# Performance work log

Measured on AMD Instinct MI355X. Metric: run time of the kernel, lower is better.

## Reference

```python
import jax, jax.numpy as jnp
import numpy as np
from jax import lax

EPS = 1e-5


def maxpool3x3(x):
    # 3x3 max pool, stride 1, pad 1 (NCHW)
    return lax.reduce_window(x, -jnp.inf, lax.max,
                             window_dimensions=(1, 1, 3, 3),
                             window_strides=(1, 1, 1, 1),
                             padding=((0, 0), (0, 0), (1, 1), (1, 1)))


def focus_downsample(x):
    B, C, H, W = x.shape
    pad_h = (3 - H % 3) % 3
    pad_w = (3 - W % 3) % 3
    if pad_h or pad_w:
        x = jnp.pad(x, ((0, 0), (0, 0), (0, pad_h), (0, pad_w)))
    return jnp.concatenate([x[..., i::3, j::3] for i in range(3) for j in range(3)], axis=1)


def batchnorm(x, gamma, beta):
    # training-mode BatchNorm2d: stats over (B,H,W)
    mean = jnp.mean(x, axis=(0, 2, 3), keepdims=True)
    var = jnp.var(x, axis=(0, 2, 3), keepdims=True)
    g = gamma.reshape(1, -1, 1, 1)
    b = beta.reshape(1, -1, 1, 1)
    return (x - mean) * jax.lax.rsqrt(var + EPS) * g + b


def dwconv(x, w, pad_h, pad_w):
    # depthwise conv, w: (C,1,kh,kw)
    return lax.conv_general_dilated(x, w, window_strides=(1, 1),
                                    padding=((pad_h, pad_h), (pad_w, pad_w)),
                                    dimension_numbers=('NCHW', 'OIHW', 'NCHW'),
                                    feature_group_count=x.shape[1])


def h_transform(x):
    B, C, H, W = x.shape
    x = jnp.pad(x, ((0, 0), (0, 0), (0, 0), (0, W)))
    x = x.reshape(B, C, -1)[..., :-W]
    return x.reshape(B, C, H, 2 * W - 1)


def inv_h_transform(x):
    B, C, H, _ = x.shape
    x = x.reshape(B, C, -1)
    x = jnp.pad(x, ((0, 0), (0, 0), (0, H)))
    x = x.reshape(B, C, H, 2 * H)
    return x[..., :H]


def v_transform(x):
    return h_transform(x.transpose(0, 1, 3, 2)).transpose(0, 1, 3, 2)


def inv_v_transform(x):
    return inv_h_transform(x.transpose(0, 1, 3, 2)).transpose(0, 1, 3, 2)


def pixel_shuffle3(x):
    B, C9, h, w = x.shape
    C = C9 // 9
    x = x.reshape(B, C, 3, 3, h, w)
    x = x.transpose(0, 1, 4, 2, 5, 3)  # B,C,h,3,w,3
    return x.reshape(B, C, 3 * h, 3 * w)


def setup_inputs() -> dict:
    key = jax.random.key(0)
    ks = jax.random.split(key, 10)
    C, K = 64, 11
    B, H, W = 16, 144, 144
    s = 0.05
    return {
        'x': jax.random.normal(ks[0], (B, C, H, W), jnp.float32),
        'w_mixer': jax.random.normal(ks[1], (9, C, C), jnp.float32) * s,
        'g_mnorm': jnp.ones((9 * C,), jnp.float32),
        'b_mnorm': jnp.zeros((9 * C,), jnp.float32),
        'w_h1': jax.random.normal(ks[2], (C, 1, K, 3), jnp.float32) * s,
        'w_v1': jax.random.normal(ks[3], (C, 1, 3, K), jnp.float32) * s,
        'w_h2': jax.random.normal(ks[4], (C, 1, K, 3), jnp.float32) * s,
        'w_v2': jax.random.normal(ks[5], (C, 1, 3, K), jnp.float32) * s,
        'g_norm': jnp.ones((C,), jnp.float32),
        'b_norm': jnp.zeros((C,), jnp.float32),
    }


def reference(x, w_mixer, g_mnorm, b_mnorm, w_h1, w_v1, w_h2, w_v2, g_norm, b_norm):
    C = w_h1.shape[0]
    K = w_h1.shape[2]
    pad = K // 2
    H, W = x.shape[-2:]

    x_pool = maxpool3x3(x)
    x_focus = focus_downsample(x_pool)               # (B,9C,H/3,W/3)

    # grouped 1x1 conv, groups=9
    B, _, h, w = x_focus.shape
    xg = x_focus.reshape(B, 9, C, h, w)
    x_mixed = jnp.einsum('goi,bgihw->bgohw', w_mixer, xg).reshape(B, 9 * C, h, w)
    x_mixed = batchnorm(x_mixed, g_mnorm, b_mnorm)

    x_tem, x_key = x_mixed[:, :C], x_mixed[:, C:]

    x_h1 = dwconv(x_tem, w_h1, pad, 1)
    x_w1 = dwconv(x_tem, w_v1, 1, pad)
    x_h2 = inv_h_transform(dwconv(h_transform(x_tem), w_h2, pad, 1))
    x_w2 = inv_v_transform(dwconv(v_transform(x_tem), w_v2, 1, pad))

    att_map = batchnorm(x_h1 + x_w1 + x_h2 + x_w2, g_norm, b_norm)
    final_features = jnp.concatenate([att_map, x_key], axis=1)
    att = pixel_shuffle3(final_features)[..., :H, :W]
    return x * jax.nn.sigmoid(att)
```

## Files before the change

kernel.cpp:

```cpp
#include <hip/hip_runtime.h>
#include <hip/hip_bf16.h>

typedef __hip_bfloat16 bf16;
typedef unsigned short us;
typedef __attribute__((ext_vector_type(8))) short short8;
typedef __attribute__((ext_vector_type(4))) float floatx4;

__device__ __forceinline__ float b2f(bf16 v){ return __bfloat162float(v); }
__device__ __forceinline__ bf16  f2b(float v){ return __float2bfloat16(v); }
__device__ __forceinline__ float ldx(const void* p, size_t i, int isf){
    return isf ? ((const float*)p)[i] : b2f(((const bf16*)p)[i]);
}
__device__ __forceinline__ us bfbits(float v){
    bf16 h = f2b(v); return *(us*)&h;
}
__device__ __forceinline__ float us2f(us u){
    unsigned int w = ((unsigned int)u)<<16; float f; __builtin_memcpy(&f,&w,4); return f;
}
__device__ __forceinline__ float uniformf(float v){
    return __int_as_float(__builtin_amdgcn_readfirstlane(__float_as_int(v)));
}

#define BB   16
#define CC   64
#define HH   144
#define WW   144
#define HS   48
#define SP   (HS*HS)
#define NTOT (BB*CC*HH*WW)
#define NCH  36864
#define INV_NCH (1.f/36864.f)

template<int TISF>
__device__ __forceinline__ int isf_of(const int* flag){
    if(TISF >= 0) return TISF;
    return *flag;
}

__global__ void k_sniff(const unsigned int* __restrict__ x, int* __restrict__ flag){
    __shared__ int hit;
    if(threadIdx.x==0) hit = 0;
    __syncthreads();
    int local = 0;
    for(int t=threadIdx.x; t<4096; t+=256){
        unsigned int w = x[t];
        if(((w>>7)&0xFFu)==0xFFu || ((w>>23)&0xFFu)==0xFFu) local = 1;
    }
    if(local) atomicOr(&hit, 1);
    __syncthreads();
    if(threadIdx.x==0) *flag = hit;
}

template<int TISF>
__global__ __launch_bounds__(256) void k_pool3(const void* __restrict__ x,
                                               us* __restrict__ pf,
                                               const int* __restrict__ flag,
                                               float* __restrict__ stats){
    __shared__ float l [18*148];
    __shared__ float hm[18*148];
    int isf = isf_of<TISF>(flag);
    int bid = blockIdx.x;
    int tid = threadIdx.x;
    if(bid==0){
        for(int i=tid; i<1280; i+=256) stats[i] = 0.f;
    }
    int strip = bid % 9;
    int bc = bid / 9;
    int b = bc>>6, c = bc&63;
    int r0 = strip*16;
    size_t base = (size_t)bc*HH*WW;
    for(int t=tid; t<18*18; t+=256){
        int row = t/18, ch = t%18;
        int rr = r0-1+row; int c0 = ch*8;
        float v[8];
        if(rr>=0 && rr<HH){
            if(isf){
                const float* xp = (const float*)x + base + (size_t)rr*WW + c0;
                float4 f0 = *(const float4*)xp;
                float4 f1 = *(const float4*)(xp+4);
                v[0]=f0.x;v[1]=f0.y;v[2]=f0.z;v[3]=f0.w;
                v[4]=f1.x;v[5]=f1.y;v[6]=f1.z;v[7]=f1.w;
            } else {
                const us* xp = (const us*)x + base + (size_t)rr*WW + c0;
                uint4 d = *(const uint4*)xp;
                const us* u = (const us*)&d;
                #pragma unroll
                for(int e=0;e<8;++e) v[e] = us2f(u[e]);
            }
        } else {
            #pragma unroll
            for(int e=0;e<8;++e) v[e] = -INFINITY;
        }
        #pragma unroll
        for(int e=0;e<8;++e) l[row*148 + c0 + e] = v[e];
    }
    __syncthreads();
    for(int t=tid; t<18*144; t+=256){
        int row = t/144, cc = t%144;
        float a = l[row*148+cc];
        float bb = (cc>0)   ? l[row*148+cc-1] : -INFINITY;
        float cv = (cc<143) ? l[row*148+cc+1] : -INFINITY;
        hm[row*148+cc] = fmaxf(a, fmaxf(bb,cv));
    }
    __syncthreads();
    for(int t=tid; t<576; t+=256){
        int row = t/36;
        int gj  = (t/12)%3;
        int xg  = t%12;
        int R = r0+row;
        int gi = R%3, y = R/3;
        union { us u[4]; uint2 v; } pk;
        #pragma unroll
        for(int e=0;e<4;++e){
            int xx = xg*4+e; int C = 3*xx+gj;
            float m = fmaxf(hm[row*148+C],
                      fmaxf(hm[(row+1)*148+C], hm[(row+2)*148+C]));
            pk.u[e] = bfbits(m);
        }
        size_t o = ((((size_t)(b*3+gi)*3+gj)*64 + c)*48 + y)*48 + xg*4;
        *(uint2*)&pf[o] = pk.v;
    }
}

template<int TISF>
__global__ __launch_bounds__(256) void k_mix3(const us* __restrict__ pf,
        const void* __restrict__ wmix, us* __restrict__ mixed,
        float* __restrict__ sum1, float* __restrict__ ss1,
        const int* __restrict__ flag){
    __shared__ __align__(16) us sAll[4096 + 288*64];
    __shared__ float sS[64], sQ[64];
    us* sW = sAll;
    us* sI = sAll + 4096;
    int isf = isf_of<TISF>(flag);
    int bid = blockIdx.x;
    int chunk = bid%8, g = (bid/8)%9, b = bid/72;
    int gi = g/3, gj = g%3;
    int tid = threadIdx.x, lane = tid&63, w = tid>>6;
    {
        int o  = tid>>2;
        int i0 = (tid&3)*16;
        us wb[16];
        if(isf){
            const float* wp = (const float*)wmix + (size_t)g*4096 + (size_t)o*64 + i0;
            #pragma unroll
            for(int e=0;e<16;e+=4){
                float4 f = *(const float4*)(wp+e);
                wb[e]=bfbits(f.x); wb[e+1]=bfbits(f.y);
                wb[e+2]=bfbits(f.z); wb[e+3]=bfbits(f.w);
            }
        } else {
            const us* wp = (const us*)wmix + (size_t)g*4096 + (size_t)o*64 + i0;
            uint4 d0 = *(const uint4*)wp, d1 = *(const uint4*)(wp+8);
            const us* u0 = (const us*)&d0; const us* u1 = (const us*)&d1;
            #pragma unroll
            for(int e=0;e<8;++e){ wb[e]=u0[e]; wb[8+e]=u1[e]; }
        }
        #pragma unroll
        for(int e=0;e<16;++e){
            int i = i0+e;
            sW[o*64 + ((((i>>3)+o)&7)<<3) + (i&7)] = wb[e];
        }
    }
    if(tid<64){ sS[tid]=0.f; sQ[tid]=0.f; }
    {
        int i = lane;
        const us* src = pf + ((((size_t)(b*3+gi)*3+gj)*64 + i)*48 + (size_t)chunk*6)*48;
        for(int vv=w*9; vv<(w+1)*9; ++vv){
            uint4 d = *(const uint4*)(src + vv*8);
            const us* u = (const us*)&d;
            #pragma unroll
            for(int e=0;e<8;++e){
                int s = vv*8+e;
                sI[s*64 + ((((i>>3)+s)&7)<<3) + (i&7)] = u[e];
            }
        }
    }
    __syncthreads();
    int n = lane&15, quad = lane>>4;
    int m = w*16 + n;
    short8 a0 = *(const short8*)&sW[m*64 + (((quad     + m)&7)<<3)];
    short8 a1 = *(const short8*)&sW[m*64 + ((((4+quad) + m)&7)<<3)];
    floatx4 acc[18];
    #pragma unroll
    for(int nt=0; nt<18; ++nt) acc[nt] = (floatx4){0.f,0.f,0.f,0.f};
    #pragma unroll
    for(int nt=0; nt<18; ++nt){
        int site = nt*16 + n;
        short8 b0 = *(const short8*)&sI[site*64 + (((quad     + site)&7)<<3)];
        short8 b1 = *(const short8*)&sI[site*64 + ((((4+quad) + site)&7)<<3)];
        acc[nt] = __builtin_amdgcn_mfma_f32_16x16x32_bf16(a0, b0, acc[nt], 0,0,0);
        acc[nt] = __builtin_amdgcn_mfma_f32_16x16x32_bf16(a1, b1, acc[nt], 0,0,0);
    }
    float s[4] = {0,0,0,0}, q[4] = {0,0,0,0};
    #pragma unroll
    for(int nt=0; nt<18; ++nt){
        #pragma unroll
        for(int r=0;r<4;++r){
            float v = acc[nt][r];
            s[r] += v; q[r] += v*v;
        }
    }
    #pragma unroll
    for(int off=1; off<=8; off<<=1){
        #pragma unroll
        for(int r=0;r<4;++r){
            s[r] += __shfl_xor(s[r], off, 64);
            q[r] += __shfl_xor(q[r], off, 64);
        }
    }
    if(n==0){
        #pragma unroll
        for(int r=0;r<4;++r){
            atomicAdd(&sS[w*16+quad*4+r], s[r]);
            atomicAdd(&sQ[w*16+quad*4+r], q[r]);
        }
    }
    __syncthreads();
    if(tid<64){
        atomicAdd(&sum1[g*64+tid], sS[tid]);
        atomicAdd(&ss1 [g*64+tid], sQ[tid]);
    }
    us* swr = sAll + w*640;
    int o_loc = lane>>2, s8 = (lane&3)*8;
    size_t rowbase = ((size_t)(b*576 + g*64 + w*16))*SP + (size_t)chunk*288;
    #pragma unroll
    for(int mp=0; mp<9; ++mp){
        __builtin_amdgcn_wave_barrier();
        #pragma unroll
        for(int half=0; half<2; ++half){
            int nt = mp*2 + half;
            #pragma unroll
            for(int r=0;r<4;++r)
                swr[(quad*4+r)*40 + half*16 + n] = bfbits(acc[nt][r]);
        }
        __builtin_amdgcn_wave_barrier();
        uint4 vv = *(const uint4*)&swr[o_loc*40 + s8];
        *(uint4*)&mixed[rowbase + (size_t)o_loc*SP + (size_t)(mp*32 + s8)] = vv;
    }
}

template<int TISF>
__global__ __launch_bounds__(256) void k_conv3(const us* __restrict__ mixed,
    const float* __restrict__ sum1, const float* __restrict__ ss1,
    const void* __restrict__ gm, const void* __restrict__ bm,
    const void* __restrict__ wh1, const void* __restrict__ wv1,
    const void* __restrict__ wh2, const void* __restrict__ wv2,
    us* __restrict__ att, float* __restrict__ sum2, float* __restrict__ ss2,
    const int* __restrict__ flag){
    __shared__ float tile[60*60+64];
    __shared__ float w1[33], w2[33], w34[39];
    __shared__ float r1[256], r2[256];
    int isf = isf_of<TISF>(flag);
    int bid = blockIdx.x;
    int b = bid/64, c = bid%64;
    int tid = threadIdx.x;
    for(int t=tid; t<3664; t+=256) tile[t] = 0.f;
    if(tid < 33){
        w1[tid] = ldx(wh1, c*33 + tid, isf);
    } else if(tid < 66){
        w2[tid-33] = ldx(wv1, c*33 + (tid-33), isf);
    } else if(tid < 105){
        int k = tid-66;
        int r = k/3 - 6;
        int vo = k%3 - 1;
        float a = 0.f;
        if(r >= -5 && r <= 5)
            a += ldx(wh2, c*33 + (r+5)*3 + (vo+1), isf);
        int u = vo - r;
        if(u >= -5 && u <= 5)
            a += ldx(wv2, c*33 + (vo+1)*11 + (u+5), isf);
        w34[k] = a;
    }
    __syncthreads();
    float mu   = sum1[c]*INV_NCH;
    float var  = ss1[c]*INV_NCH - mu*mu;
    float is   = rsqrtf(var + 1e-5f)*ldx(gm,c,isf);
    float be   = ldx(bm,c,isf);
    const us* src = mixed + (size_t)(b*576 + c)*SP;
    float w1r[33], w2r[33], w34r[39];
    #pragma unroll
    for(int i=0;i<33;++i) w1r[i] = uniformf(w1[i]);
    #pragma unroll
    for(int i=0;i<33;++i) w2r[i] = uniformf(w2[i]);
    #pragma unroll
    for(int i=0;i<39;++i) w34r[i] = w34[i];
    for(int t=tid; t<288; t+=256){
        int h = t/6, w0 = (t%6)*8;
        uint4 d = *(const uint4*)(src + t*8);
        const us* u = (const us*)&d;
        #pragma unroll
        for(int e=0;e<8;++e)
            tile[(h+6)*60 + (w0+6) + e] = (us2f(u[e]) - mu)*is + be;
    }
    __syncthreads();
    const int cg = tid & 15, rg = tid >> 4;
    const int W0 = cg*3, H0 = rg*3;
    const float* tb = &tile[(H0+6)*60 + (W0+6)];
    float acc[3][3] = {{0.f,0.f,0.f},{0.f,0.f,0.f},{0.f,0.f,0.f}};
    #pragma unroll
    for(int ry=-1; ry<=3; ++ry){
        float R[13];
        #pragma unroll
        for(int k=0;k<13;++k) R[k] = tb[ry*60 + (k-5)];
        #pragma unroll
        for(int dy=0; dy<3; ++dy){
            if(ry-dy < -1 || ry-dy > 1) continue;
            #pragma unroll
            for(int dc=0; dc<3; ++dc)
                #pragma unroll
                for(int v=-5; v<=5; ++v)
                    acc[dy][dc] += w2r[(ry-dy+1)*11 + (v+5)] * R[dc+v+5];
        }
    }
    #pragma unroll
    for(int ry=-5; ry<=7; ++ry){
        float R[5];
        #pragma unroll
        for(int k=0;k<5;++k) R[k] = tb[ry*60 + (k-1)];
        #pragma unroll
        for(int dy=0; dy<3; ++dy){
            if(ry-dy < -5 || ry-dy > 5) continue;
            #pragma unroll
            for(int dc=0; dc<3; ++dc)
                #pragma unroll
                for(int v=-1; v<=1; ++v)
                    acc[dy][dc] += w1r[(ry-dy+5)*3 + (v+1)] * R[dc+v+1];
        }
    }
    #pragma unroll
    for(int ry=-6; ry<=8; ++ry){
        const int dyLo = (ry-6 > 0) ? ry-6 : 0;
        const int dyHi = (ry+6 < 2) ? ry+6 : 2;
        const int jLo  = (dyLo - ry) - 1;
        float R[7];
        #pragma unroll
        for(int k=0;k<7;++k) R[k] = tb[ry*60 + jLo + k];
        #pragma unroll
        for(int dy=0; dy<3; ++dy){
            if(dy < dyLo || dy > dyHi) continue;
            #pragma unroll
            for(int dc=0; dc<3; ++dc)
                #pragma unroll
                for(int v=-1; v<=1; ++v)
                    acc[dy][dc] += w34r[(ry-dy+6)*3 + (v+1)] * R[(dy-ry)+dc+v - jLo];
        }
    }
    us* out = att + (size_t)(b*64 + c)*SP;
    float sl = 0.f, ql = 0.f;
    #pragma unroll
    for(int dy=0; dy<3; ++dy)
        #pragma unroll
        for(int dc=0; dc<3; ++dc){
            float a = acc[dy][dc];
            out[(H0+dy)*48 + W0+dc] = bfbits(a);
            sl += a; ql += a*a;
        }
    r1[tid]=sl; r2[tid]=ql; __syncthreads();
    for(int o=128;o>0;o>>=1){
        if(tid<o){ r1[tid]+=r1[tid+o]; r2[tid]+=r2[tid+o]; }
        __syncthreads();
    }
    if(tid==0){
        atomicAdd(&sum2[c], r1[0]);
        atomicAdd(&ss2 [c], r2[0]);
    }
}

template<int TISF>
__global__ __launch_bounds__(256) void k_final3(const void* __restrict__ x,
    const us* __restrict__ mixed, const us* __restrict__ att,
    const void* __restrict__ gm, const void* __restrict__ bm,
    const void* __restrict__ gn, const void* __restrict__ bnb,
    const float* __restrict__ sum1, const float* __restrict__ ss1,
    const float* __restrict__ sum2, const float* __restrict__ ss2,
    void* __restrict__ out, const int* __restrict__ flag){
    __shared__ __align__(16) us sT[9*1152];
    __shared__ float scs[9], shs[9];
    int isf = isf_of<TISF>(flag);
    int bid = blockIdx.x;
    int half = bid&1, c = (bid>>1)&63, b = bid>>7;
    int yy0 = half*24;
    int tid = threadIdx.x;
    if(tid < 9){
        int f = 9*c + tid;
        float sraw, qraw, gg, bb2;
        if(f < 64){ sraw = sum2[f]; qraw = ss2[f]; gg = ldx(gn,f,isf);  bb2 = ldx(bnb,f,isf); }
        else      { sraw = sum1[f]; qraw = ss1[f]; gg = ldx(gm,f,isf);  bb2 = ldx(bm,f,isf); }
        float mm  = sraw*INV_NCH;
        float ist = rsqrtf(qraw*INV_NCH - mm*mm + 1e-5f);
        float sc = ist*gg;
        scs[tid] = sc;
        shs[tid] = bb2 - mm*sc;
    }
    for(int t=tid; t<9*144; t+=256){
        int j = t/144, qq = t%144;
        int f = 9*c + j;
        const us* srcp = ((f<64) ? att   + (size_t)(b*64 +f)*SP
                                 : mixed + (size_t)(b*576+f)*SP) + yy0*48;
        ((uint4*)&sT[j*1152])[qq] = ((const uint4*)srcp)[qq];
    }
    __syncthreads();
    size_t pbase = (size_t)(b*64+c)*HH*WW;
    for(int t=tid; t<1296; t+=256){
        int Yl = t/18;
        int Xb = (t%18)*8;
        int yyl = Yl/3, r = Yl%3;
        float vo[8];
        #pragma unroll
        for(int k=0;k<8;++k){
            int X = Xb+k;
            int xx = X/3, sph = X%3;
            int j = 3*r + sph;
            float raw = us2f(sT[j*1152 + yyl*48 + xx]);
            float v = raw*scs[j] + shs[j];
            vo[k] = 1.f/(1.f + __expf(-v));
        }
        size_t off = pbase + (size_t)(yy0*3 + Yl)*WW + Xb;
        if(isf){
            const float4* xp = (const float4*)((const float*)x + off);
            float4 x0 = xp[0], x1 = xp[1];
            float4 o0, o1;
            o0.x = x0.x*vo[0]; o0.y = x0.y*vo[1]; o0.z = x0.z*vo[2]; o0.w = x0.w*vo[3];
            o1.x = x1.x*vo[4]; o1.y = x1.y*vo[5]; o1.z = x1.z*vo[6]; o1.w = x1.w*vo[7];
            float4* op = (float4*)((float*)out + off);
            op[0] = o0; op[1] = o1;
        } else {
            uint4 xr = *(const uint4*)((const us*)x + off);
            const us* xu = (const us*)&xr;
            union { us u[8]; uint4 v; } pk;
            #pragma unroll
            for(int k=0;k<8;++k)
                pk.u[k] = bfbits(us2f(xu[k])*vo[k]);
            *(uint4*)((us*)out + off) = pk.v;
        }
    }
}


extern "C" void kernel_launch(void* const* d_in, const int* in_sizes, int n_in,
                              void* d_out, int out_size, void* d_ws, size_t ws_size,
                              hipStream_t stream) {
    (void)n_in; (void)out_size; (void)ws_size;
    const void* x    = d_in[0];
    const void* wmix = d_in[1];
    const void* gm   = d_in[2];
    const void* bm   = d_in[3];
    const void* wh1  = d_in[4];
    const void* wv1  = d_in[5];
    const void* wh2  = d_in[6];
    const void* wv2  = d_in[7];
    const void* gn   = d_in[8];
    const void* bnb  = d_in[9];

    us* pf = (us*)d_out;
    char* ws = (char*)d_ws;
    us*    mixed = (us*)   (ws + 0);
    us*    att   = (us*)   (ws + 42467328);
    float* st1a  = (float*)(ws + 47185920);
    float* st1b  = (float*)(ws + 47188224);
    float* st2a  = (float*)(ws + 47190528);
    float* st2b  = (float*)(ws + 47190784);
    int*   flag  = (int*)  (ws + 47191040);

    int isf;
    if(in_sizes[0] == (int)((long long)NTOT*4)) isf = 1;
    else if(in_sizes[0] == (int)((long long)NTOT*2)) isf = 0;
    else isf = -1;

    if(isf < 0)
        k_sniff<<<1, 256, 0, stream>>>((const unsigned int*)x, flag);

#define LAUNCH_ALL(T)                                                          \
    k_pool3<T><<<BB*CC*9, 256, 0, stream>>>(x, pf, flag, st1a);                \
    k_mix3<T><<<BB*9*8, 256, 0, stream>>>(pf, wmix, mixed, st1a, st1b, flag);  \
    k_conv3<T><<<BB*64, 256, 0, stream>>>(mixed, st1a, st1b, gm, bm,           \
                                          wh1, wv1, wh2, wv2, att,             \
                                          st2a, st2b, flag);                   \
    k_final3<T><<<BB*CC*2, 256, 0, stream>>>(x, mixed, att, gm, bm, gn, bnb,   \
                                             st1a, st1b, st2a, st2b, d_out, flag);

    if(isf == 1)      { LAUNCH_ALL(1)  }
    else if(isf == 0) { LAUNCH_ALL(0)  }
    else              { LAUNCH_ALL(-1) }
#undef LAUNCH_ALL
}
```

Baseline: 246.4 us.

## Enlarge pool strips, store bf16 in LDS, vectorize pooling, use shuffle reductions

The maxpool kernel now handles 48-row strips instead of 16, which cuts redundant halo row loads. It keeps tiles in shared memory as bf16 rather than float and does the horizontal and vertical max passes with 8-wide vector loads, so the focus gather becomes a plain strided copy. The conv kernel replaces its shared-memory tree reduction with wave shuffles plus one atomic per wave. The trade-off is fewer blocks for the pool kernel and four times as many atomics in conv. Rounding fp32 input to bf16 before the max is order-preserving, so results should not change.

```diff
diff --git a/kernel.cpp b/kernel.cpp
--- a/kernel.cpp
+++ b/kernel.cpp
@@ -30,6 +30,7 @@
 #define NTOT (BB*CC*HH*WW)
 #define NCH  36864
 #define INV_NCH (1.f/36864.f)
+#define NINF_US 0xFF80u
 
 template<int TISF>
 __device__ __forceinline__ int isf_of(const int* flag){
@@ -56,67 +57,88 @@
                                                us* __restrict__ pf,
                                                const int* __restrict__ flag,
                                                float* __restrict__ stats){
-    __shared__ float l [18*148];
-    __shared__ float hm[18*148];
+    __shared__ __align__(16) us l [50*152];
+    __shared__ __align__(16) us hm[50*152];
     int isf = isf_of<TISF>(flag);
     int bid = blockIdx.x;
     int tid = threadIdx.x;
     if(bid==0){
         for(int i=tid; i<1280; i+=256) stats[i] = 0.f;
     }
-    int strip = bid % 9;
-    int bc = bid / 9;
+    int strip = bid % 3;
+    int bc = bid / 3;
     int b = bc>>6, c = bc&63;
-    int r0 = strip*16;
+    int r0 = strip*48;
     size_t base = (size_t)bc*HH*WW;
-    for(int t=tid; t<18*18; t+=256){
+    for(int t=tid; t<50*18; t+=256){
         int row = t/18, ch = t%18;
         int rr = r0-1+row; int c0 = ch*8;
-        float v[8];
+        uint4 pk;
         if(rr>=0 && rr<HH){
             if(isf){
                 const float* xp = (const float*)x + base + (size_t)rr*WW + c0;
                 float4 f0 = *(const float4*)xp;
                 float4 f1 = *(const float4*)(xp+4);
-                v[0]=f0.x;v[1]=f0.y;v[2]=f0.z;v[3]=f0.w;
-                v[4]=f1.x;v[5]=f1.y;v[6]=f1.z;v[7]=f1.w;
+                union { us u[8]; uint4 v; } q;
+                q.u[0]=bfbits(f0.x); q.u[1]=bfbits(f0.y);
+                q.u[2]=bfbits(f0.z); q.u[3]=bfbits(f0.w);
+                q.u[4]=bfbits(f1.x); q.u[5]=bfbits(f1.y);
+                q.u[6]=bfbits(f1.z); q.u[7]=bfbits(f1.w);
+                pk = q.v;
             } else {
-                const us* xp = (const us*)x + base + (size_t)rr*WW + c0;
-                uint4 d = *(const uint4*)xp;
-                const us* u = (const us*)&d;
-                #pragma unroll
-                for(int e=0;e<8;++e) v[e] = us2f(u[e]);
+                pk = *(const uint4*)((const us*)x + base + (size_t)rr*WW + c0);
             }
         } else {
-            #pragma unroll
-            for(int e=0;e<8;++e) v[e] = -INFINITY;
-        }
-        #pragma unroll
-        for(int e=0;e<8;++e) l[row*148 + c0 + e] = v[e];
-    }
-    __syncthreads();
-    for(int t=tid; t<18*144; t+=256){
-        int row = t/144, cc = t%144;
-        float a = l[row*148+cc];
-        float bb = (cc>0)   ? l[row*148+cc-1] : -INFINITY;
-        float cv = (cc<143) ? l[row*148+cc+1] : -INFINITY;
-        hm[row*148+cc] = fmaxf(a, fmaxf(bb,cv));
-    }
-    __syncthreads();
-    for(int t=tid; t<576; t+=256){
+            pk.x = pk.y = pk.z = pk.w = 0xFF80FF80u;
+        }
+        *(uint4*)&l[row*152 + c0] = pk;
+    }
+    __syncthreads();
+    for(int t=tid; t<50*18; t+=256){
+        int row = t/18, c0 = (t%18)*8;
+        const us* lr = &l[row*152];
+        uint4 ctr = *(const uint4*)&lr[c0];
+        const us* cu = (const us*)&ctr;
+        float v[8];
+        #pragma unroll
+        for(int e=0;e<8;++e) v[e] = us2f(cu[e]);
+        float lf = (c0>0)   ? us2f(lr[c0-1]) : -INFINITY;
+        float rf = (c0<136) ? us2f(lr[c0+8]) : -INFINITY;
+        union { us u[8]; uint4 w; } q;
+        #pragma unroll
+        for(int e=0;e<8;++e){
+            float a = (e==0) ? lf : v[e-1];
+            float bb= (e==7) ? rf : v[e+1];
+            q.u[e] = bfbits(fmaxf(v[e], fmaxf(a,bb)));
+        }
+        *(uint4*)&hm[row*152 + c0] = q.w;
+    }
+    __syncthreads();
+    for(int t=tid; t<48*18; t+=256){
+        int row = t/18, c0 = (t%18)*8;
+        uint4 a = *(const uint4*)&hm[ row   *152 + c0];
+        uint4 bq= *(const uint4*)&hm[(row+1)*152 + c0];
+        uint4 cq= *(const uint4*)&hm[(row+2)*152 + c0];
+        const us* au = (const us*)&a;
+        const us* bu = (const us*)&bq;
+        const us* cu = (const us*)&cq;
+        union { us u[8]; uint4 w; } q;
+        #pragma unroll
+        for(int e=0;e<8;++e)
+            q.u[e] = bfbits(fmaxf(us2f(au[e]), fmaxf(us2f(bu[e]), us2f(cu[e]))));
+        *(uint4*)&l[row*152 + c0] = q.w;
+    }
+    __syncthreads();
+    for(int t=tid; t<48*36; t+=256){
         int row = t/36;
         int gj  = (t/12)%3;
         int xg  = t%12;
-        int R = r0+row;
-        int gi = R%3, y = R/3;
+        int gi = row%3, y = strip*16 + row/3;
+        const us* vr = &l[row*152];
         union { us u[4]; uint2 v; } pk;
         #pragma unroll
-        for(int e=0;e<4;++e){
-            int xx = xg*4+e; int C = 3*xx+gj;
-            float m = fmaxf(hm[row*148+C],
-                      fmaxf(hm[(row+1)*148+C], hm[(row+2)*148+C]));
-            pk.u[e] = bfbits(m);
-        }
+        for(int e=0;e<4;++e)
+            pk.u[e] = vr[3*(xg*4+e) + gj];
         size_t o = ((((size_t)(b*3+gi)*3+gj)*64 + c)*48 + y)*48 + xg*4;
         *(uint2*)&pf[o] = pk.v;
     }
@@ -249,7 +271,6 @@
     const int* __restrict__ flag){
     __shared__ float tile[60*60+64];
     __shared__ float w1[33], w2[33], w34[39];
-    __shared__ float r1[256], r2[256];
     int isf = isf_of<TISF>(flag);
     int bid = blockIdx.x;
     int b = bid/64, c = bid%64;
@@ -355,14 +376,14 @@
             out[(H0+dy)*48 + W0+dc] = bfbits(a);
             sl += a; ql += a*a;
         }
-    r1[tid]=sl; r2[tid]=ql; __syncthreads();
-    for(int o=128;o>0;o>>=1){
-        if(tid<o){ r1[tid]+=r1[tid+o]; r2[tid]+=r2[tid+o]; }
-        __syncthreads();
-    }
-    if(tid==0){
-        atomicAdd(&sum2[c], r1[0]);
-        atomicAdd(&ss2 [c], r2[0]);
+    #pragma unroll
+    for(int off=1; off<=32; off<<=1){
+        sl += __shfl_xor(sl, off, 64);
+        ql += __shfl_xor(ql, off, 64);
+    }
+    if((tid&63)==0){
+        atomicAdd(&sum2[c], sl);
+        atomicAdd(&ss2 [c], ql);
     }
 }
 
@@ -471,7 +492,7 @@
         k_sniff<<<1, 256, 0, stream>>>((const unsigned int*)x, flag);
 
 #define LAUNCH_ALL(T)                                                          \
-    k_pool3<T><<<BB*CC*9, 256, 0, stream>>>(x, pf, flag, st1a);                \
+    k_pool3<T><<<BB*CC*3, 256, 0, stream>>>(x, pf, flag, st1a);                \
     k_mix3<T><<<BB*9*8, 256, 0, stream>>>(pf, wmix, mixed, st1a, st1b, flag);  \
     k_conv3<T><<<BB*64, 256, 0, stream>>>(mixed, st1a, st1b, gm, bm,           \
                                           wh1, wv1, wh2, wv2, att,             \
```

Measured after the change: 264.4 us. 1.07x slower.

## Split depthwise conv kernel into half-plane blocks with wave-shuffle stats reduction

Applied to the files above, without the earlier changes.

The conv stage now launches two 128-thread blocks per (batch, channel) plane, each covering 24 output rows with a smaller halo tile, instead of one 256-thread block per plane. The shared-memory tree reduction for the BN statistics is replaced by a wave-level shuffle reduction with one atomic per wave, and the readfirstlane weight broadcast is removed. This is meant to double the block count and cut LDS use and barrier overhead. In exchange, the halo rows are loaded twice and there are more atomics per channel.

```diff
diff --git a/kernel.cpp b/kernel.cpp
--- a/kernel.cpp
+++ b/kernel.cpp
@@ -16,9 +16,6 @@
 }
 __device__ __forceinline__ float us2f(us u){
     unsigned int w = ((unsigned int)u)<<16; float f; __builtin_memcpy(&f,&w,4); return f;
-}
-__device__ __forceinline__ float uniformf(float v){
-    return __int_as_float(__builtin_amdgcn_readfirstlane(__float_as_int(v)));
 }
 
 #define BB   16
@@ -240,21 +237,22 @@
 }
 
 template<int TISF>
-__global__ __launch_bounds__(256) void k_conv3(const us* __restrict__ mixed,
+__global__ __launch_bounds__(128, 2) void k_conv3(const us* __restrict__ mixed,
     const float* __restrict__ sum1, const float* __restrict__ ss1,
     const void* __restrict__ gm, const void* __restrict__ bm,
     const void* __restrict__ wh1, const void* __restrict__ wv1,
     const void* __restrict__ wh2, const void* __restrict__ wv2,
     us* __restrict__ att, float* __restrict__ sum2, float* __restrict__ ss2,
     const int* __restrict__ flag){
-    __shared__ float tile[60*60+64];
+    __shared__ float tile[36*60 + 16];
     __shared__ float w1[33], w2[33], w34[39];
-    __shared__ float r1[256], r2[256];
     int isf = isf_of<TISF>(flag);
     int bid = blockIdx.x;
-    int b = bid/64, c = bid%64;
+    int half = bid & 1;
+    int bc = bid >> 1;
+    int b = bc/64, c = bc%64;
     int tid = threadIdx.x;
-    for(int t=tid; t<3664; t+=256) tile[t] = 0.f;
+    for(int t=tid; t<36*60+16; t+=128) tile[t] = 0.f;
     if(tid < 33){
         w1[tid] = ldx(wh1, c*33 + tid, isf);
     } else if(tid < 66){
@@ -276,32 +274,36 @@
     float var  = ss1[c]*INV_NCH - mu*mu;
     float is   = rsqrtf(var + 1e-5f)*ldx(gm,c,isf);
     float be   = ldx(bm,c,isf);
+    float w1r[33], w2r[33], w34r[39];
+    #pragma unroll
+    for(int i=0;i<33;++i) w1r[i] = w1[i];
+    #pragma unroll
+    for(int i=0;i<33;++i) w2r[i] = w2[i];
+    #pragma unroll
+    for(int i=0;i<39;++i) w34r[i] = w34[i];
     const us* src = mixed + (size_t)(b*576 + c)*SP;
-    float w1r[33], w2r[33], w34r[39];
-    #pragma unroll
-    for(int i=0;i<33;++i) w1r[i] = uniformf(w1[i]);
-    #pragma unroll
-    for(int i=0;i<33;++i) w2r[i] = uniformf(w2[i]);
-    #pragma unroll
-    for(int i=0;i<39;++i) w34r[i] = w34[i];
-    for(int t=tid; t<288; t+=256){
-        int h = t/6, w0 = (t%6)*8;
-        uint4 d = *(const uint4*)(src + t*8);
-        const us* u = (const us*)&d;
-        #pragma unroll
-        for(int e=0;e<8;++e)
-            tile[(h+6)*60 + (w0+6) + e] = (us2f(u[e]) - mu)*is + be;
+    int g0 = half*24 - 6;
+    for(int t=tid; t<216; t+=128){
+        int lr = t/6, w0 = (t%6)*8;
+        int gr = g0 + lr;
+        if(gr >= 0 && gr < 48){
+            uint4 d = *(const uint4*)(src + gr*48 + w0);
+            const us* u = (const us*)&d;
+            #pragma unroll
+            for(int e=0;e<8;++e)
+                tile[lr*60 + 6 + w0 + e] = (us2f(u[e]) - mu)*is + be;
+        }
     }
     __syncthreads();
     const int cg = tid & 15, rg = tid >> 4;
     const int W0 = cg*3, H0 = rg*3;
-    const float* tb = &tile[(H0+6)*60 + (W0+6)];
+    const float* tb = &tile[H0*60 + W0];
     float acc[3][3] = {{0.f,0.f,0.f},{0.f,0.f,0.f},{0.f,0.f,0.f}};
     #pragma unroll
     for(int ry=-1; ry<=3; ++ry){
         float R[13];
         #pragma unroll
-        for(int k=0;k<13;++k) R[k] = tb[ry*60 + (k-5)];
+        for(int k=0;k<13;++k) R[k] = tb[(6+ry)*60 + 1 + k];
         #pragma unroll
         for(int dy=0; dy<3; ++dy){
             if(ry-dy < -1 || ry-dy > 1) continue;
@@ -316,7 +318,7 @@
     for(int ry=-5; ry<=7; ++ry){
         float R[5];
         #pragma unroll
-        for(int k=0;k<5;++k) R[k] = tb[ry*60 + (k-1)];
+        for(int k=0;k<5;++k) R[k] = tb[(6+ry)*60 + 5 + k];
         #pragma unroll
         for(int dy=0; dy<3; ++dy){
             if(ry-dy < -5 || ry-dy > 5) continue;
@@ -334,7 +336,7 @@
         const int jLo  = (dyLo - ry) - 1;
         float R[7];
         #pragma unroll
-        for(int k=0;k<7;++k) R[k] = tb[ry*60 + jLo + k];
+        for(int k=0;k<7;++k) R[k] = tb[(6+ry)*60 + 6 + jLo + k];
         #pragma unroll
         for(int dy=0; dy<3; ++dy){
             if(dy < dyLo || dy > dyHi) continue;
@@ -346,23 +348,24 @@
         }
     }
     us* out = att + (size_t)(b*64 + c)*SP;
+    int rowg = half*24 + H0;
     float sl = 0.f, ql = 0.f;
     #pragma unroll
     for(int dy=0; dy<3; ++dy)
         #pragma unroll
         for(int dc=0; dc<3; ++dc){
             float a = acc[dy][dc];
-            out[(H0+dy)*48 + W0+dc] = bfbits(a);
+            out[(rowg+dy)*48 + W0+dc] = bfbits(a);
             sl += a; ql += a*a;
         }
-    r1[tid]=sl; r2[tid]=ql; __syncthreads();
-    for(int o=128;o>0;o>>=1){
-        if(tid<o){ r1[tid]+=r1[tid+o]; r2[tid]+=r2[tid+o]; }
-        __syncthreads();
-    }
-    if(tid==0){
-        atomicAdd(&sum2[c], r1[0]);
-        atomicAdd(&ss2 [c], r2[0]);
+    #pragma unroll
+    for(int off=1; off<=32; off<<=1){
+        sl += __shfl_xor(sl, off, 64);
+        ql += __shfl_xor(ql, off, 64);
+    }
+    if((tid&63)==0){
+        atomicAdd(&sum2[c], sl);
+        atomicAdd(&ss2 [c], ql);
     }
 }
 
@@ -473,9 +476,9 @@
 #define LAUNCH_ALL(T)                                                          \
     k_pool3<T><<<BB*CC*9, 256, 0, stream>>>(x, pf, flag, st1a);                \
     k_mix3<T><<<BB*9*8, 256, 0, stream>>>(pf, wmix, mixed, st1a, st1b, flag);  \
-    k_conv3<T><<<BB*64, 256, 0, stream>>>(mixed, st1a, st1b, gm, bm,           \
-                                          wh1, wv1, wh2, wv2, att,             \
-                                          st2a, st2b, flag);                   \
+    k_conv3<T><<<BB*64*2, 128, 0, stream>>>(mixed, st1a, st1b, gm, bm,         \
+                                            wh1, wv1, wh2, wv2, att,           \
+                                            st2a, st2b, flag);                 \
     k_final3<T><<<BB*CC*2, 256, 0, stream>>>(x, mixed, att, gm, bm, gn, bnb,   \
                                              st1a, st1b, st2a, st2b, d_out, flag);
 
```

Measured after the change: 260.4 us. 5.7% more time.
